# Performance work log

Measured on AMD Instinct MI355X. Metric: run time of the kernel, lower is better.

The kernel has to match this reference:

```python
import jax, jax.numpy as jnp
import numpy as np

DROPOUT_P = 0.1
EMBED = 128  # head dim; inv_scale_factor = sqrt(EMBED)


def setup_inputs() -> dict:
    key = jax.random.key(0)
    ks = jax.random.split(key, 9)
    B, S, H, D = 4, 2048, 16, EMBED
    mk = lambda k, shape: jax.random.normal(k, shape, dtype=jnp.float32)
    return {
        "query": mk(ks[0], (B, S, H, D)),
        "key": mk(ks[1], (B, S, H, D)),
        "value": mk(ks[2], (B, S, H, D)),
        "Wq": mk(ks[3], (D, D)) / np.sqrt(D),
        "bq": mk(ks[4], (D,)) * 0.01,
        "Wk": mk(ks[5], (D, D)) / np.sqrt(D),
        "bk": mk(ks[6], (D,)) * 0.01,
        "Wv": mk(ks[7], (D, D)) / np.sqrt(D),
        "bv": mk(ks[8], (D,)) * 0.01,
    }


def reference(query, key, value, Wq, bq, Wk, bk, Wv, bv):
    # Linear (torch convention: x @ W.T + b) then permute(0,2,1,3): [B,S,H,D] -> [B,H,S,D]
    q = (query @ Wq.T + bq).transpose(0, 2, 1, 3)
    k = (key @ Wk.T + bk).transpose(0, 2, 1, 3)
    v = (value @ Wv.T + bv).transpose(0, 2, 1, 3)
    scale = 1.0 / jnp.sqrt(jnp.float32(EMBED))  # div by embed_size**0.5
    scores = jnp.einsum("bhqd,bhkd->bhqk", q, k) * scale
    probs = jax.nn.softmax(scores, axis=-1)
    # deterministic inverted dropout with fixed key (train-mode dropout)
    keep = jax.random.bernoulli(jax.random.key(42), 1.0 - DROPOUT_P, probs.shape)
    probs = jnp.where(keep, probs / (1.0 - DROPOUT_P), 0.0)
    return jnp.einsum("bhqk,bhkd->bhqd", probs, v)
```

## Files before the change

### kernel.cpp

```cpp
#include <hip/hip_runtime.h>
#include <stdint.h>

#define BB 4
#define SS 2048
#define HH 16
#define DD 128

typedef __attribute__((ext_vector_type(8))) short bf16x8;
typedef __attribute__((ext_vector_type(4))) float f32x4;

__device__ __forceinline__ float bf2f(uint16_t u) {
  union { uint32_t i; float f; } x; x.i = ((uint32_t)u) << 16; return x.f;
}
__device__ __forceinline__ uint16_t f2bf(float f) {
  union { float f; uint32_t i; } u; u.f = f;
  uint32_t r = u.i + 0x7FFFu + ((u.i >> 16) & 1u);
  return (uint16_t)(r >> 16);
}

#define TF_C 3865470464u
#define TF_ROUND(r) { x0 += x1; x1 = __builtin_amdgcn_alignbit(x1, x1, 32 - (r)) ^ x0; }

__device__ __forceinline__ void tf2x32(uint32_t k0, uint32_t k1, uint32_t c0, uint32_t c1,
                                       uint32_t& o0, uint32_t& o1) {
  const uint32_t k2 = 0x1BD11BDAu ^ k0 ^ k1;
  uint32_t x0 = c0 + k0, x1 = c1 + k1;
  TF_ROUND(13) TF_ROUND(15) TF_ROUND(26) TF_ROUND(6)
  x0 += k1; x1 += k2 + 1u;
  TF_ROUND(17) TF_ROUND(29) TF_ROUND(16) TF_ROUND(24)
  x0 += k2; x1 += k0 + 2u;
  TF_ROUND(13) TF_ROUND(15) TF_ROUND(26) TF_ROUND(6)
  x0 += k0; x1 += k1 + 3u;
  TF_ROUND(17) TF_ROUND(29) TF_ROUND(16) TF_ROUND(24)
  x0 += k1; x1 += k2 + 4u;
  TF_ROUND(13) TF_ROUND(15) TF_ROUND(26) TF_ROUND(6)
  x0 += k2; x1 += k0 + 5u;
  o0 = x0; o1 = x1;
}

__device__ __forceinline__ uint32_t tf_bit_part(uint32_t i) {
  uint32_t o0, o1;
  tf2x32(0u, 42u, 0u, i, o0, o1);
  return ((o0 ^ o1) < TF_C) ? 1u : 0u;
}

__global__ void detect_kernel(const uint16_t* __restrict__ q, int* __restrict__ flag) {
  if (blockIdx.x == 0 && threadIdx.x == 0) {
    int ok = 1;
    for (int i = 0; i < 64; ++i) {
      float a = fabsf(bf2f(q[2 * i]));
      if (!(a == 0.0f || (a > 9.0e-13f && a < 64.0f))) ok = 0;
    }
    *flag = ok;
  }
}

__global__ __launch_bounds__(256) void proj_kernel(
    const void* __restrict__ xq, const void* __restrict__ xk, const void* __restrict__ xv,
    const void* __restrict__ Wq, const void* __restrict__ bq,
    const void* __restrict__ Wk, const void* __restrict__ bk,
    const void* __restrict__ Wv, const void* __restrict__ bv,
    uint16_t* __restrict__ Qo, uint16_t* __restrict__ Ko, uint16_t* __restrict__ Vo,
    const int* __restrict__ flag) {
  const int isbf = *flag;
  const int tz = blockIdx.y;
  const void* x = (tz == 0) ? xq : (tz == 1) ? xk : xv;
  const void* W = (tz == 0) ? Wq : (tz == 1) ? Wk : Wv;
  const void* bs = (tz == 0) ? bq : (tz == 1) ? bk : bv;
  uint16_t* out = (tz == 0) ? Qo : (tz == 1) ? Ko : Vo;
  const int vtrans = (tz == 2);

  const int wave = threadIdx.x >> 6, lane = threadIdx.x & 63;
  const int c = lane & 15, quad = lane >> 4;
  const int m0 = blockIdx.x * 64 + wave * 16;
  const int mrow = m0 + c;

  bf16x8 af[4];
  if (isbf) {
    const uint16_t* xr = (const uint16_t*)x + (size_t)mrow * DD + quad * 8;
#pragma unroll
    for (int t = 0; t < 4; ++t) af[t] = *(const bf16x8*)(xr + t * 32);
  } else {
    const float* xr = (const float*)x + (size_t)mrow * DD + quad * 8;
#pragma unroll
    for (int t = 0; t < 4; ++t) {
#pragma unroll
      for (int j = 0; j < 8; ++j) af[t][j] = (short)f2bf(xr[t * 32 + j]);
    }
  }

  size_t obase[4];
#pragma unroll
  for (int r = 0; r < 4; ++r) {
    int m = m0 + quad * 4 + r;
    int b = m >> 15;
    int s = (m >> 4) & (SS - 1);
    int h = m & (HH - 1);
    obase[r] = vtrans ? ((size_t)(b * HH + h) * SS * DD + (size_t)(s >> 5) * (DD * 32) + (s & 31))
                      : (((size_t)(b * HH + h) * SS + (size_t)s) * DD);
  }

  for (int nt = 0; nt < 8; ++nt) {
    f32x4 acc = {0.f, 0.f, 0.f, 0.f};
    const int n = nt * 16 + c;
    if (isbf) {
      const uint16_t* wr = (const uint16_t*)W + (size_t)n * DD + quad * 8;
#pragma unroll
      for (int t = 0; t < 4; ++t)
        acc = __builtin_amdgcn_mfma_f32_16x16x32_bf16(af[t], *(const bf16x8*)(wr + t * 32), acc, 0, 0, 0);
    } else {
      const float* wr = (const float*)W + (size_t)n * DD + quad * 8;
#pragma unroll
      for (int t = 0; t < 4; ++t) {
        bf16x8 bfr;
#pragma unroll
        for (int j = 0; j < 8; ++j) bfr[j] = (short)f2bf(wr[t * 32 + j]);
        acc = __builtin_amdgcn_mfma_f32_16x16x32_bf16(af[t], bfr, acc, 0, 0, 0);
      }
    }
    const float bias = isbf ? bf2f(((const uint16_t*)bs)[n]) : ((const float*)bs)[n];
#pragma unroll
    for (int r = 0; r < 4; ++r) {
      float v = acc[r] + bias;
      size_t o = obase[r] + (vtrans ? (size_t)n * 32 : (size_t)n);
      out[o] = f2bf(v);
    }
  }
}

__global__ __launch_bounds__(256, 4) void attn_kernel(
    const uint16_t* __restrict__ Q, const uint16_t* __restrict__ K, const uint16_t* __restrict__ Vt,
    void* __restrict__ outv, const int* __restrict__ flag) {
  __shared__ __align__(16) uint16_t Ks[2][32][128];
  __shared__ __align__(16) uint16_t Vs[2][128][32];
  __shared__ __align__(16) uint16_t pl[4][16][40];
  const int isbf = *flag;
  const int tid = threadIdx.x;
  const int wave = tid >> 6, lane = tid & 63;
  const int c = lane & 15, quad = lane >> 4;
  const int bh = blockIdx.x >> 5;
  const int q0 = (blockIdx.x & 31) * 64 + wave * 16;

  const uint16_t* Qb = Q + (size_t)bh * SS * DD;
  const uint16_t* Kb = K + (size_t)bh * SS * DD;
  const uint16_t* Vb = Vt + (size_t)bh * SS * DD;

  bf16x8 qf[4];
  {
    const uint16_t* qr = Qb + (q0 + c) * DD + quad * 8;
#pragma unroll
    for (int t = 0; t < 4; ++t) qf[t] = *(const bf16x8*)(qr + t * 32);
  }

  const f32x4 zero = {0.f, 0.f, 0.f, 0.f};
  f32x4 o[8];
#pragma unroll
  for (int i = 0; i < 8; ++i) o[i] = zero;
  float lsum[4] = {0.f, 0.f, 0.f, 0.f};

  const float sc2 = 0.12751744f;

  uint32_t ibase[4];
#pragma unroll
  for (int r = 0; r < 4; ++r)
    ibase[r] = ((uint32_t)bh * SS + (uint32_t)(q0 + quad * 4 + r)) * SS + (uint32_t)c;

  uint16_t(*plw)[40] = pl[wave];

  const int krow = tid >> 4;
  const int kd0 = krow * 256 + (((tid & 15) * 16) ^ ((krow & 7) << 4));
  const int kd1 = kd0 + 16 * 256;
  const int vd0 = tid * 16, vd1 = vd0 + 4096;
  const uint16_t* kga = Kb + krow * DD + (tid & 15) * 8;
  const uint16_t* vga = Vb + tid * 8;

  bf16x8 ksa = *(const bf16x8*)(kga);
  bf16x8 ksb = *(const bf16x8*)(kga + 16 * DD);
  bf16x8 vsa = *(const bf16x8*)(vga);
  bf16x8 vsb = *(const bf16x8*)(vga + 2048);
  {
    char* kd = (char*)Ks[0]; *(bf16x8*)(kd + kd0) = ksa; *(bf16x8*)(kd + kd1) = ksb;
    char* vd = (char*)Vs[0]; *(bf16x8*)(vd + vd0) = vsa; *(bf16x8*)(vd + vd1) = vsb;
  }
  __syncthreads();

  const int ksw = (c & 7) << 4;
  int cur = 0;

  for (int kt = 0; kt < SS / 32; ++kt) {
    const int ktn = (kt + 1) & 63;
    ksa = *(const bf16x8*)(kga + ktn * 32 * DD);
    ksb = *(const bf16x8*)(kga + ktn * 32 * DD + 16 * DD);
    vsa = *(const bf16x8*)(vga + ktn * 4096);
    vsb = *(const bf16x8*)(vga + ktn * 4096 + 2048);

    const char* klds = (const char*)Ks[cur];
    f32x4 sf[2];
#pragma unroll
    for (int ks = 0; ks < 2; ++ks) {
      f32x4 acc = zero;
      const char* kr = klds + (ks * 16 + c) * 256;
#pragma unroll
      for (int t = 0; t < 4; ++t) {
        bf16x8 kf = *(const bf16x8*)(kr + ((quad * 16 + t * 64) ^ ksw));
        acc = __builtin_amdgcn_mfma_f32_16x16x32_bf16(qf[t], kf, acc, 0, 0, 0);
      }
      sf[ks] = acc;
    }
    const uint32_t ik = (uint32_t)kt * 32u;
#pragma unroll
    for (int ks = 0; ks < 2; ++ks) {
#pragma unroll
      for (int r = 0; r < 4; ++r) {
        float p = __builtin_amdgcn_exp2f(sf[ks][r] * sc2);
        lsum[r] += p;
        uint32_t b0, b1;
        tf2x32(0u, 42u, 0u, ibase[r] + ik + (uint32_t)(ks * 16), b0, b1);
        float pm = ((b0 ^ b1) < TF_C) ? p : 0.0f;
        plw[quad * 4 + r][ks * 16 + c] = f2bf(pm);
      }
    }
    bf16x8 pa = *(const bf16x8*)(&plw[c][quad * 8]);
    const char* vlds = (const char*)Vs[cur] + c * 64 + quad * 16;
#pragma unroll
    for (int dt = 0; dt < 8; ++dt) {
      bf16x8 vf = *(const bf16x8*)(vlds + dt * 1024);
      o[dt] = __builtin_amdgcn_mfma_f32_16x16x32_bf16(pa, vf, o[dt], 0, 0, 0);
    }

    {
      char* kd = (char*)Ks[cur ^ 1]; *(bf16x8*)(kd + kd0) = ksa; *(bf16x8*)(kd + kd1) = ksb;
      char* vd = (char*)Vs[cur ^ 1]; *(bf16x8*)(vd + vd0) = vsa; *(bf16x8*)(vd + vd1) = vsb;
    }
    __syncthreads();
    cur ^= 1;
  }

#pragma unroll
  for (int r = 0; r < 4; ++r) {
    float v = lsum[r];
    v += __shfl_xor(v, 1);
    v += __shfl_xor(v, 2);
    v += __shfl_xor(v, 4);
    v += __shfl_xor(v, 8);
    lsum[r] = 1.0f / (0.9f * v);
  }

  const size_t ob = (size_t)bh * SS * DD;
  if (isbf) {
    uint16_t* outp = (uint16_t*)outv;
#pragma unroll
    for (int dt = 0; dt < 8; ++dt)
#pragma unroll
      for (int r = 0; r < 4; ++r)
        outp[ob + (size_t)(q0 + quad * 4 + r) * DD + dt * 16 + c] = f2bf(o[dt][r] * lsum[r]);
  } else {
    float* outp = (float*)outv;
#pragma unroll
    for (int dt = 0; dt < 8; ++dt)
#pragma unroll
      for (int r = 0; r < 4; ++r)
        outp[ob + (size_t)(q0 + quad * 4 + r) * DD + dt * 16 + c] = o[dt][r] * lsum[r];
  }

  if (blockIdx.x == 0 && wave == 0) {
    uint32_t o0, o1;
    tf2x32(0u, 0u, 0u, 0u, o0, o1);
    bool bad1 = (o0 != 0x6b200159u) || (o1 != 0x99ba4efeu);
#pragma unroll
    for (int ks = 0; ks < 2; ++ks)
#pragma unroll
      for (int r = 0; r < 4; ++r)
        plw[quad * 4 + r][ks * 16 + c] = f2bf((float)((quad * 4 + r) * 32 + ks * 16 + c));
    bf16x8 tp = *(const bf16x8*)(&plw[c][quad * 8]);
    bool bad3 = false;
#pragma unroll
    for (int j = 0; j < 8; ++j)
      bad3 |= ((uint16_t)tp[j] != f2bf((float)(c * 32 + quad * 8 + j)));
    bf16x8 ta, tb;
#pragma unroll
    for (int j = 0; j < 8; ++j) {
      ta[j] = (short)f2bf((float)(c * 32 + quad * 8 + j));
      tb[j] = (short)((quad * 8 + j == c) ? f2bf(1.0f) : 0);
    }
    f32x4 tc = zero;
    tc = __builtin_amdgcn_mfma_f32_16x16x32_bf16(ta, tb, tc, 0, 0, 0);
    bool bad4 = false;
#pragma unroll
    for (int r = 0; r < 4; ++r)
      bad4 |= (tc[r] != bf2f(f2bf((float)((quad * 4 + r) * 32 + c))));
#pragma unroll
    for (int j = 0; j < 8; ++j) {
      ta[j] = (short)((quad * 8 + j == c) ? f2bf(1.0f) : 0);
      tb[j] = (short)f2bf((float)(c * 32 + quad * 8 + j));
    }
    f32x4 td = zero;
    td = __builtin_amdgcn_mfma_f32_16x16x32_bf16(ta, tb, td, 0, 0, 0);
    bool bad5 = false;
#pragma unroll
    for (int r = 0; r < 4; ++r)
      bad5 |= (td[r] != bf2f(f2bf((float)(c * 32 + quad * 4 + r))));
    float main_d0 = __shfl(o[0][0] * lsum[0], 0);
    float main_d64 = __shfl(o[4][0] * lsum[0], 0);
    float a0 = 0.f, a64 = 0.f, al = 0.f;
    for (int k = lane; k < SS; k += 64) {
      float s = 0.f;
      for (int d = 0; d < DD; ++d) s += bf2f(Qb[d]) * bf2f(Kb[k * DD + d]);
      float p = __builtin_amdgcn_exp2f(s * sc2);
      al += p;
      if (tf_bit_part((uint32_t)k)) {
        a0 += p * bf2f(Vb[(size_t)(k >> 5) * 4096 + (k & 31)]);
        a64 += p * bf2f(Vb[(size_t)(k >> 5) * 4096 + 64 * 32 + (k & 31)]);
      }
    }
#pragma unroll
    for (int off = 32; off; off >>= 1) {
      a0 += __shfl_xor(a0, off);
      a64 += __shfl_xor(a64, off);
      al += __shfl_xor(al, off);
    }
    bool bad6 = (fabsf(a0 / (0.9f * al) - main_d0) > 0.02f) ||
                (fabsf(a64 / (0.9f * al) - main_d64) > 0.02f);

    unsigned long long m1 = __ballot(bad1), m3 = __ballot(bad3),
                       m4 = __ballot(bad4), m5 = __ballot(bad5), m6 = __ballot(bad6);
    if (lane == 0) {
      float s = 0.f;
      if (m1) s = 1e8f;
      else if (m3) s = 1e6f;
      else if (m4) s = 1e5f;
      else if (m5) s = 4e4f;
      else if (m6) s = 2e4f;
      if (s != 0.f) {
        if (isbf) ((uint16_t*)outv)[0] = f2bf(s);
        else ((float*)outv)[0] = s;
      }
    }
  }
}

extern "C" void kernel_launch(void* const* d_in, const int* in_sizes, int n_in,
                              void* d_out, int out_size, void* d_ws, size_t ws_size,
                              hipStream_t stream) {
  char* ws = (char*)d_ws;
  int* flag = (int*)ws;
  uint16_t* Qo = (uint16_t*)(ws + 256);
  uint16_t* Ko = Qo + (size_t)BB * HH * SS * DD;
  uint16_t* Vo = Ko + (size_t)BB * HH * SS * DD;

  hipLaunchKernelGGL(detect_kernel, dim3(1), dim3(64), 0, stream,
                     (const uint16_t*)d_in[0], flag);
  hipLaunchKernelGGL(proj_kernel, dim3(2048, 3), dim3(256), 0, stream,
                     d_in[0], d_in[1], d_in[2], d_in[3], d_in[4], d_in[5], d_in[6], d_in[7], d_in[8],
                     Qo, Ko, Vo, flag);
  hipLaunchKernelGGL(attn_kernel, dim3(2048), dim3(256), 0, stream,
                     Qo, Ko, Vo, d_out, flag);
}
```

Measured before the change: 1.152 ms.

## Stage weights in LDS, coalesce projection stores, swizzle V tile in attention

The projection kernel now loads each W matrix once into swizzled shared memory and reads MFMA fragments from LDS instead of global memory. Each block maps to one (b,h) and 64 sequence rows. Outputs are staged in a per-wave LDS buffer so Q/K/V are written as 16-byte vector stores rather than scattered 2-byte stores. In the attention kernel the V shared-memory tile gets an XOR swizzle to reduce bank conflicts on fragment reads. The cost is extra shared memory and a barrier in the projection, plus a lower occupancy hint on that kernel.

```diff
diff --git a/kernel.cpp b/kernel.cpp
--- a/kernel.cpp
+++ b/kernel.cpp
@@ -55,13 +55,15 @@
   }
 }
 
-__global__ __launch_bounds__(256) void proj_kernel(
+__global__ __launch_bounds__(256, 3) void proj_kernel(
     const void* __restrict__ xq, const void* __restrict__ xk, const void* __restrict__ xv,
     const void* __restrict__ Wq, const void* __restrict__ bq,
     const void* __restrict__ Wk, const void* __restrict__ bk,
     const void* __restrict__ Wv, const void* __restrict__ bv,
     uint16_t* __restrict__ Qo, uint16_t* __restrict__ Ko, uint16_t* __restrict__ Vo,
     const int* __restrict__ flag) {
+  __shared__ __align__(16) uint16_t Wl[128 * 128];
+  __shared__ __align__(16) char Tep[4][5120];
   const int isbf = *flag;
   const int tz = blockIdx.y;
   const void* x = (tz == 0) ? xq : (tz == 1) ? xk : xv;
@@ -70,60 +72,96 @@
   uint16_t* out = (tz == 0) ? Qo : (tz == 1) ? Ko : Vo;
   const int vtrans = (tz == 2);
 
-  const int wave = threadIdx.x >> 6, lane = threadIdx.x & 63;
+  const int tid = threadIdx.x;
+  const int wave = tid >> 6, lane = tid & 63;
   const int c = lane & 15, quad = lane >> 4;
-  const int m0 = blockIdx.x * 64 + wave * 16;
-  const int mrow = m0 + c;
+  const int bh = blockIdx.x >> 5;
+  const int s0 = (blockIdx.x & 31) * 64;
+  const int sw = s0 + wave * 16;
+  const int b = bh >> 4, h = bh & 15;
+
+  {
+    const int row = tid >> 1;
+    const int cb = (tid & 1) * 8;
+    char* wl = (char*)Wl + row * 256;
+    if (isbf) {
+      const uint16_t* wr = (const uint16_t*)W + (size_t)row * DD + (tid & 1) * 64;
+#pragma unroll
+      for (int i = 0; i < 8; ++i) {
+        bf16x8 v = *(const bf16x8*)(wr + i * 8);
+        *(bf16x8*)(wl + ((((cb + i) << 4)) ^ ((row & 7) << 4))) = v;
+      }
+    } else {
+      const float* wr = (const float*)W + (size_t)row * DD + (tid & 1) * 64;
+#pragma unroll
+      for (int i = 0; i < 8; ++i) {
+        bf16x8 v;
+#pragma unroll
+        for (int j = 0; j < 8; ++j) v[j] = (short)f2bf(wr[i * 8 + j]);
+        *(bf16x8*)(wl + ((((cb + i) << 4)) ^ ((row & 7) << 4))) = v;
+      }
+    }
+  }
 
   bf16x8 af[4];
-  if (isbf) {
-    const uint16_t* xr = (const uint16_t*)x + (size_t)mrow * DD + quad * 8;
-#pragma unroll
-    for (int t = 0; t < 4; ++t) af[t] = *(const bf16x8*)(xr + t * 32);
-  } else {
-    const float* xr = (const float*)x + (size_t)mrow * DD + quad * 8;
-#pragma unroll
-    for (int t = 0; t < 4; ++t) {
-#pragma unroll
-      for (int j = 0; j < 8; ++j) af[t][j] = (short)f2bf(xr[t * 32 + j]);
-    }
-  }
-
-  size_t obase[4];
-#pragma unroll
-  for (int r = 0; r < 4; ++r) {
-    int m = m0 + quad * 4 + r;
-    int b = m >> 15;
-    int s = (m >> 4) & (SS - 1);
-    int h = m & (HH - 1);
-    obase[r] = vtrans ? ((size_t)(b * HH + h) * SS * DD + (size_t)(s >> 5) * (DD * 32) + (s & 31))
-                      : (((size_t)(b * HH + h) * SS + (size_t)s) * DD);
-  }
+  {
+    const size_t xrow = ((size_t)(b * SS + sw + c) * HH + h) * DD;
+    if (isbf) {
+      const uint16_t* xr = (const uint16_t*)x + xrow + quad * 8;
+#pragma unroll
+      for (int t = 0; t < 4; ++t) af[t] = *(const bf16x8*)(xr + t * 32);
+    } else {
+      const float* xr = (const float*)x + xrow + quad * 8;
+#pragma unroll
+      for (int t = 0; t < 4; ++t) {
+#pragma unroll
+        for (int j = 0; j < 8; ++j) af[t][j] = (short)f2bf(xr[t * 32 + j]);
+      }
+    }
+  }
+  __syncthreads();
+
+  char* myT = Tep[wave];
+  uint16_t* tq = (uint16_t*)myT;
 
   for (int nt = 0; nt < 8; ++nt) {
     f32x4 acc = {0.f, 0.f, 0.f, 0.f};
     const int n = nt * 16 + c;
-    if (isbf) {
-      const uint16_t* wr = (const uint16_t*)W + (size_t)n * DD + quad * 8;
-#pragma unroll
-      for (int t = 0; t < 4; ++t)
-        acc = __builtin_amdgcn_mfma_f32_16x16x32_bf16(af[t], *(const bf16x8*)(wr + t * 32), acc, 0, 0, 0);
+    const char* wb = (char*)Wl + n * 256;
+    const int nsw = (c & 7) << 4;
+#pragma unroll
+    for (int t = 0; t < 4; ++t) {
+      bf16x8 wf = *(const bf16x8*)(wb + (((quad + t * 4) << 4) ^ nsw));
+      acc = __builtin_amdgcn_mfma_f32_16x16x32_bf16(af[t], wf, acc, 0, 0, 0);
+    }
+    const float bias = isbf ? bf2f(((const uint16_t*)bs)[n]) : ((const float*)bs)[n];
+    if (!vtrans) {
+#pragma unroll
+      for (int r = 0; r < 4; ++r)
+        tq[(quad * 4 + r) * 136 + n] = f2bf(acc[r] + bias);
     } else {
-      const float* wr = (const float*)W + (size_t)n * DD + quad * 8;
-#pragma unroll
-      for (int t = 0; t < 4; ++t) {
-        bf16x8 bfr;
-#pragma unroll
-        for (int j = 0; j < 8; ++j) bfr[j] = (short)f2bf(wr[t * 32 + j]);
-        acc = __builtin_amdgcn_mfma_f32_16x16x32_bf16(af[t], bfr, acc, 0, 0, 0);
-      }
-    }
-    const float bias = isbf ? bf2f(((const uint16_t*)bs)[n]) : ((const float*)bs)[n];
-#pragma unroll
-    for (int r = 0; r < 4; ++r) {
-      float v = acc[r] + bias;
-      size_t o = obase[r] + (vtrans ? (size_t)n * 32 : (size_t)n);
-      out[o] = f2bf(v);
+      uint32_t p01 = (uint32_t)f2bf(acc[0] + bias) | ((uint32_t)f2bf(acc[1] + bias) << 16);
+      uint32_t p23 = (uint32_t)f2bf(acc[2] + bias) | ((uint32_t)f2bf(acc[3] + bias) << 16);
+      *(uint64_t*)(myT + n * 40 + quad * 8) = (uint64_t)p01 | ((uint64_t)p23 << 32);
+    }
+  }
+
+  if (!vtrans) {
+    const size_t rb = (size_t)(bh * SS + sw + c) * DD;
+#pragma unroll
+    for (int p = 0; p < 4; ++p) {
+      const int ch = quad + 4 * p;
+      bf16x8 v = *(const bf16x8*)(myT + c * 272 + ch * 16);
+      *(bf16x8*)(out + rb + ch * 8) = v;
+    }
+  } else {
+    const size_t vb = (size_t)bh * (SS * DD);
+#pragma unroll
+    for (int p = 0; p < 4; ++p) {
+      const int d = p * 32 + (lane >> 1), oct = lane & 1;
+      bf16x8 v = *(const bf16x8*)(myT + d * 40 + oct * 16);
+      const int sg = s0 + wave * 16 + oct * 8;
+      *(bf16x8*)(out + vb + (size_t)(sg >> 5) * 4096 + d * 32 + (sg & 31)) = v;
     }
   }
 }
@@ -170,7 +208,8 @@
   const int krow = tid >> 4;
   const int kd0 = krow * 256 + (((tid & 15) * 16) ^ ((krow & 7) << 4));
   const int kd1 = kd0 + 16 * 256;
-  const int vd0 = tid * 16, vd1 = vd0 + 4096;
+  const int vswz = ((tid >> 3) & 3) << 4;
+  const int vd0 = (tid * 16) ^ vswz, vd1 = vd0 + 4096;
   const uint16_t* kga = Kb + krow * DD + (tid & 15) * 8;
   const uint16_t* vga = Vb + tid * 8;
 
@@ -185,6 +224,7 @@
   __syncthreads();
 
   const int ksw = (c & 7) << 4;
+  const int vr0 = (c * 64 + quad * 16) ^ ((((c >> 1) & 3)) << 4);
   int cur = 0;
 
   for (int kt = 0; kt < SS / 32; ++kt) {
@@ -221,7 +261,7 @@
       }
     }
     bf16x8 pa = *(const bf16x8*)(&plw[c][quad * 8]);
-    const char* vlds = (const char*)Vs[cur] + c * 64 + quad * 16;
+    const char* vlds = (const char*)Vs[cur] + vr0;
 #pragma unroll
     for (int dt = 0; dt < 8; ++dt) {
       bf16x8 vf = *(const bf16x8*)(vlds + dt * 1024);
```

New measurement: 972.6 us. -15.6%, faster.
